# Kernel optimization log

Measured on AMD Instinct MI355X. Metric: run time of the kernel, lower is better.

Reference implementation:

```python
import jax, jax.numpy as jnp
import numpy as np

D_EMBED = 1024
N_HEADS = 16
D_HEAD = 64
D_MLP = 4096
SEQ = 2048
BATCH = 2
ALPHA = 1.0


def setup_inputs() -> dict:
    key = jax.random.key(0)
    ks = jax.random.split(key, 7)
    s = ALPHA / np.sqrt(D_EMBED)
    return {
        "x": jax.random.normal(ks[0], (BATCH, SEQ, D_EMBED), jnp.float32),
        "W_K": s * jax.random.normal(ks[1], (N_HEADS, D_HEAD, D_EMBED), jnp.float32),
        "W_Q": s * jax.random.normal(ks[2], (N_HEADS, D_HEAD, D_EMBED), jnp.float32),
        "W_V": s * jax.random.normal(ks[3], (N_HEADS, D_HEAD, D_EMBED), jnp.float32),
        "W_O": s * jax.random.normal(ks[4], (D_EMBED, N_HEADS * D_HEAD), jnp.float32),
        "W_in": s * jax.random.normal(ks[5], (D_MLP, D_EMBED), jnp.float32),
        "b_in": jnp.zeros((D_MLP,), jnp.float32),
        "W_out": s * jax.random.normal(ks[6], (D_EMBED, D_MLP), jnp.float32),
        "b_out": jnp.zeros((D_EMBED,), jnp.float32),
    }


def reference(x, W_K, W_Q, W_V, W_O, W_in, b_in, W_out, b_out):
    b, c_len, _ = x.shape
    d_head = W_K.shape[1]
    # q/k/v: [batch, head, ctx, d_head]
    k = jnp.einsum('ahe,bce->bach', W_K, x)
    q = jnp.einsum('ahe,bce->bach', W_Q, x)
    v = jnp.einsum('ahe,bce->bach', W_V, x)
    # scores[b,a,c,C] = k_c . q_C  (faithful to original index convention)
    scores = jnp.einsum('bach,baCh->bacC', k, q)
    mask = jnp.tril(jnp.ones((c_len, c_len), dtype=x.dtype))  # [c, C]
    masked = scores * mask - 1e10 * (1.0 - mask)
    attn = jax.nn.softmax(masked / np.sqrt(d_head), axis=-1)  # softmax over C (query idx)
    # z[b,a,C,h] = sum_c v[b,a,c,h] * attn[b,a,c,C]
    z = jnp.einsum('bach,bacC->baCh', v, attn)
    z_flat = jnp.transpose(z, (0, 2, 1, 3)).reshape(b, c_len, -1)  # [b, c, a*h]
    attn_out = jnp.einsum('ef,bcf->bce', W_O, z_flat)
    x = x + attn_out
    h = jnp.einsum('me,bce->bcm', W_in, x) + b_in
    h = jax.nn.relu(h)
    mlp_out = jnp.einsum('em,bcm->bce', W_out, h) + b_out
    return x + mlp_out
```

## Files before the change

kernel.cpp:

```cpp
#include <hip/hip_runtime.h>
#include <hip/hip_bf16.h>
#include <cstdint>
#include <cstddef>

typedef __bf16 bf16;
typedef bf16 bf16x4 __attribute__((ext_vector_type(4)));
typedef bf16 bf16x8 __attribute__((ext_vector_type(8)));
typedef float floatx4 __attribute__((ext_vector_type(4)));

#define MFMA16(a, b, c) __builtin_amdgcn_mfma_f32_16x16x32_bf16((a), (b), (c), 0, 0, 0)

#define K2 0.18033688011112042f

__device__ __forceinline__ void async16(const void* g, void* l) {
    __builtin_amdgcn_global_load_lds((const __attribute__((address_space(1))) void*)g,
                                     (__attribute__((address_space(3))) void*)l,
                                     16, 0, 0);
}

__device__ __forceinline__ void stage64(const bf16* g0, int ldg, bf16* lds, int wave, int lane) {
#pragma unroll
    for (int i = 0; i < 2; ++i) {
        int r0 = wave * 16 + i * 8;
        async16(g0 + (size_t)(r0 + (lane >> 3)) * ldg + (lane & 7) * 8,
                lds + r0 * 64);
    }
}

#define BAR_VM()                                              \
    do {                                                      \
        asm volatile("s_waitcnt vmcnt(0)" ::: "memory");      \
        __builtin_amdgcn_s_barrier();                         \
    } while (0)
#define BAR_LGKM()                                            \
    do {                                                      \
        asm volatile("s_waitcnt lgkmcnt(0)" ::: "memory");    \
        __builtin_amdgcn_s_barrier();                         \
    } while (0)

__global__ __launch_bounds__(256) void cvt_all(const float* __restrict__ x,
                                               const float* __restrict__ WQ,
                                               const float* __restrict__ WK,
                                               const float* __restrict__ WV,
                                               const float* __restrict__ WO,
                                               const float* __restrict__ Win,
                                               const float* __restrict__ Wout,
                                               bf16* __restrict__ xb,
                                               bf16* __restrict__ wqkv,
                                               bf16* __restrict__ wo,
                                               bf16* __restrict__ win,
                                               bf16* __restrict__ wout) {
    int blk = blockIdx.x;
    const float* src;
    bf16* dst;
    int off;
    if (blk < 1024)      { src = WQ;   dst = wqkv;           off = blk; }
    else if (blk < 2048) { src = WK;   dst = wqkv + 1048576; off = blk - 1024; }
    else if (blk < 3072) { src = WV;   dst = wqkv + 2097152; off = blk - 2048; }
    else if (blk < 4096) { src = WO;   dst = wo;             off = blk - 3072; }
    else if (blk < 8192) { src = Win;  dst = win;            off = blk - 4096; }
    else if (blk < 12288){ src = Wout; dst = wout;           off = blk - 8192; }
    else                 { src = x;    dst = xb;             off = blk - 12288; }
    int i = off * 1024 + threadIdx.x * 4;
    float4 v = *(const float4*)(src + i);
    bf16x4 o = {(bf16)v.x, (bf16)v.y, (bf16)v.z, (bf16)v.w};
    *(bf16x4*)(dst + i) = o;
}

template <int EPI, int NT>
__global__ __launch_bounds__(256) void gemm_dbuf(const bf16* __restrict__ A, int lda,
                                                 const bf16* __restrict__ B, int ldb, int K,
                                                 float* __restrict__ Cf, bf16* __restrict__ Cb,
                                                 int ldc, const float* __restrict__ bias,
                                                 const float* __restrict__ res) {
    constexpr int NACC = NT / 32;
    __shared__ __align__(16) bf16 As[2][128 * 32];
    __shared__ __align__(16) bf16 Bs[2][NT * 32];
    const int tid = threadIdx.x, wave = tid >> 6, lane = tid & 63;
    const int m0 = blockIdx.y * 128, n0 = blockIdx.x * NT;
    const int wm = (wave >> 1) * 64, wn = (wave & 1) * (NT / 2);
    const int col = lane & 15, quad = lane >> 4;

    floatx4 acc[4][NACC];
#pragma unroll
    for (int mi = 0; mi < 4; ++mi)
#pragma unroll
        for (int ni = 0; ni < NACC; ++ni) acc[mi][ni] = (floatx4){0.f, 0.f, 0.f, 0.f};

    auto stage = [&](int buf, int k0) {
#pragma unroll
        for (int i = 0; i < 2; ++i) {
            int r0 = wave * 32 + i * 16;
            async16(A + (size_t)(m0 + r0 + (lane >> 2)) * lda + k0 + (lane & 3) * 8,
                    As[buf] + r0 * 32);
        }
        if constexpr (NT == 128) {
#pragma unroll
            for (int i = 0; i < 2; ++i) {
                int r0 = wave * 32 + i * 16;
                async16(B + (size_t)(n0 + r0 + (lane >> 2)) * ldb + k0 + (lane & 3) * 8,
                        Bs[buf] + r0 * 32);
            }
        } else {
            int r0 = wave * 16;
            async16(B + (size_t)(n0 + r0 + (lane >> 2)) * ldb + k0 + (lane & 3) * 8,
                    Bs[buf] + r0 * 32);
        }
    };

    stage(0, 0);
    const int nk = K / 32;
    for (int it = 0; it < nk; ++it) {
        __syncthreads();
        if (it + 1 < nk) stage((it + 1) & 1, (it + 1) * 32);
        const int cur = it & 1;
        bf16x8 af[4], bfr[NACC];
#pragma unroll
        for (int mi = 0; mi < 4; ++mi)
            af[mi] = *(const bf16x8*)&As[cur][(wm + mi * 16 + col) * 32 + quad * 8];
#pragma unroll
        for (int ni = 0; ni < NACC; ++ni)
            bfr[ni] = *(const bf16x8*)&Bs[cur][(wn + ni * 16 + col) * 32 + quad * 8];
#pragma unroll
        for (int mi = 0; mi < 4; ++mi)
#pragma unroll
            for (int ni = 0; ni < NACC; ++ni)
                acc[mi][ni] = MFMA16(af[mi], bfr[ni], acc[mi][ni]);
    }

#pragma unroll
    for (int mi = 0; mi < 4; ++mi)
#pragma unroll
        for (int ni = 0; ni < NACC; ++ni)
#pragma unroll
            for (int r = 0; r < 4; ++r) {
                int row = m0 + wm + mi * 16 + quad * 4 + r;
                int cc = n0 + wn + ni * 16 + col;
                size_t idx = (size_t)row * ldc + cc;
                float v = acc[mi][ni][r];
                if constexpr (EPI == 0) {
                    Cb[idx] = (bf16)v;
                } else if constexpr (EPI == 1) {
                    v += res[idx];
                    Cf[idx] = v;
                    Cb[idx] = (bf16)v;
                } else if constexpr (EPI == 2) {
                    v += bias[cc];
                    v = fmaxf(v, 0.f);
                    Cb[idx] = (bf16)v;
                } else {
                    v += bias[cc] + Cf[idx];
                    Cf[idx] = v;
                }
            }
}

__global__ __launch_bounds__(256) void transpose_v(const bf16* __restrict__ qkv,
                                                   bf16* __restrict__ vt) {
    __shared__ bf16 t[64][65];
    const int bh = blockIdx.y, ct = blockIdx.x;
    const int b = bh >> 4, a = bh & 15;
    for (int idx = threadIdx.x; idx < 4096; idx += 256) {
        int c = idx >> 6, h = idx & 63;
        t[h][c] = qkv[(size_t)(b * 2048 + ct * 64 + c) * 3072 + 2048 + a * 64 + h];
    }
    __syncthreads();
    for (int idx = threadIdx.x; idx < 4096; idx += 256) {
        int h = idx >> 6, c = idx & 63;
        vt[(size_t)(bh * 64 + h) * 2048 + ct * 64 + c] = t[h][c];
    }
}

__global__ __launch_bounds__(256) void attn_stats(const bf16* __restrict__ qkv,
                                                  float* __restrict__ mp2) {
    __shared__ __align__(16) bf16 Kt[64 * 64];
    __shared__ __align__(16) bf16 Qt[2][64 * 64];
    const int xx = blockIdx.x;
    const int ct = (xx & 1) ? (31 - (xx >> 1)) : (xx >> 1);
    const int bh = blockIdx.y;
    const int b = bh >> 4, a = bh & 15;
    const int tid = threadIdx.x, wave = tid >> 6, lane = tid & 63;
    const int col = lane & 15, quad = lane >> 4;
    const bf16* base = qkv + (size_t)b * 2048 * 3072;

    stage64(base + (size_t)ct * 64 * 3072 + 1024 + a * 64, 3072, Kt, wave, lane);
    stage64(base + a * 64, 3072, Qt[0], wave, lane);

    float lrun[4] = {0.f, 0.f, 0.f, 0.f};
    bf16x8 a0, a1;

    for (int Ct = 0; Ct <= ct; ++Ct) {
        __syncthreads();
        if (Ct < ct)
            stage64(base + (size_t)(Ct + 1) * 64 * 3072 + a * 64, 3072,
                    Qt[(Ct + 1) & 1], wave, lane);
        if (Ct == 0) {
            a0 = *(const bf16x8*)&Kt[(wave * 16 + col) * 64 + quad * 8];
            a1 = *(const bf16x8*)&Kt[(wave * 16 + col) * 64 + 32 + quad * 8];
        }
        const bf16* q = Qt[Ct & 1];
#pragma unroll
        for (int nt = 0; nt < 4; ++nt) {
            bf16x8 b0 = *(const bf16x8*)&q[(nt * 16 + col) * 64 + quad * 8];
            bf16x8 b1 = *(const bf16x8*)&q[(nt * 16 + col) * 64 + 32 + quad * 8];
            floatx4 sacc = (floatx4){0.f, 0.f, 0.f, 0.f};
            sacc = MFMA16(a0, b0, sacc);
            sacc = MFMA16(a1, b1, sacc);
#pragma unroll
            for (int r = 0; r < 4; ++r) {
                float e = __builtin_amdgcn_exp2f(sacc[r] * K2);
                if (Ct == ct && (nt * 16 + col) > (wave * 16 + quad * 4 + r)) e = 0.f;
                lrun[r] += e;
            }
        }
    }
#pragma unroll
    for (int r = 0; r < 4; ++r) {
        float t = lrun[r];
        t += __shfl_xor(t, 1);
        t += __shfl_xor(t, 2);
        t += __shfl_xor(t, 4);
        t += __shfl_xor(t, 8);
        lrun[r] = t;
    }
    if (col == 0) {
#pragma unroll
        for (int r = 0; r < 4; ++r) {
            int c = ct * 64 + wave * 16 + quad * 4 + r;
            mp2[(size_t)bh * 2048 + c] = __builtin_amdgcn_logf(lrun[r]);
        }
    }
}

__global__ __launch_bounds__(256) void attn_av(const bf16* __restrict__ qkv,
                                               const bf16* __restrict__ vt,
                                               const float* __restrict__ mp2,
                                               bf16* __restrict__ zb) {
    __shared__ __align__(16) bf16 Qt[64 * 64];
    __shared__ __align__(16) bf16 Kt[2][64 * 64];
    __shared__ __align__(16) bf16 Vt[2][64 * 64];
    __shared__ __align__(16) bf16 Pt[64 * 72];
    const int xx = blockIdx.x;
    const int Ctile = (xx & 1) ? (31 - (xx >> 1)) : (xx >> 1);
    const int bh = blockIdx.y;
    const int b = bh >> 4, a = bh & 15;
    const int tid = threadIdx.x, wave = tid >> 6, lane = tid & 63;
    const int col = lane & 15, quad = lane >> 4;
    const bf16* base = qkv + (size_t)b * 2048 * 3072;
    const float* mpb = mp2 + (size_t)bh * 2048;

    stage64(base + (size_t)Ctile * 64 * 3072 + a * 64, 3072, Qt, wave, lane);
    stage64(base + (size_t)Ctile * 64 * 3072 + 1024 + a * 64, 3072, Kt[0], wave, lane);
    stage64(vt + (size_t)bh * 64 * 2048 + Ctile * 64, 2048, Vt[0], wave, lane);

    float4 mp_cur = *(const float4*)&mpb[Ctile * 64 + wave * 16 + quad * 4];

    floatx4 zacc[4];
#pragma unroll
    for (int mi = 0; mi < 4; ++mi) zacc[mi] = (floatx4){0.f, 0.f, 0.f, 0.f};
    bf16x8 qf0[4], qf1[4];

    for (int ct = Ctile; ct < 32; ++ct) {
        const int cur = (ct - Ctile) & 1;
        BAR_VM();
        if (ct + 1 < 32) {
            stage64(base + (size_t)(ct + 1) * 64 * 3072 + 1024 + a * 64, 3072,
                    Kt[cur ^ 1], wave, lane);
            stage64(vt + (size_t)bh * 64 * 2048 + (ct + 1) * 64, 2048,
                    Vt[cur ^ 1], wave, lane);
        }
        if (ct == Ctile) {
#pragma unroll
            for (int nt = 0; nt < 4; ++nt) {
                qf0[nt] = *(const bf16x8*)&Qt[(nt * 16 + col) * 64 + quad * 8];
                qf1[nt] = *(const bf16x8*)&Qt[(nt * 16 + col) * 64 + 32 + quad * 8];
            }
        }
        bf16x8 a0 = *(const bf16x8*)&Kt[cur][(wave * 16 + col) * 64 + quad * 8];
        bf16x8 a1 = *(const bf16x8*)&Kt[cur][(wave * 16 + col) * 64 + 32 + quad * 8];

        const float mpl[4] = {mp_cur.x, mp_cur.y, mp_cur.z, mp_cur.w};
#pragma unroll
        for (int nt = 0; nt < 4; ++nt) {
            floatx4 sacc = (floatx4){0.f, 0.f, 0.f, 0.f};
            sacc = MFMA16(a0, qf0[nt], sacc);
            sacc = MFMA16(a1, qf1[nt], sacc);
            bf16x4 pv;
#pragma unroll
            for (int r = 0; r < 4; ++r) {
                float p;
                if (ct == Ctile && (nt * 16 + col) > (wave * 16 + quad * 4 + r))
                    p = 0.f;
                else
                    p = __builtin_amdgcn_exp2f(sacc[r] * K2 - mpl[r]);
                pv[r] = (bf16)p;
            }
            *(bf16x4*)&Pt[(nt * 16 + col) * 72 + wave * 16 + quad * 4] = pv;
        }
        BAR_LGKM();

        float4 mp_nxt = mp_cur;
        if (ct + 1 < 32)
            mp_nxt = *(const float4*)&mpb[(ct + 1) * 64 + wave * 16 + quad * 4];

        bf16x8 v0 = *(const bf16x8*)&Vt[cur][(wave * 16 + col) * 64 + quad * 8];
        bf16x8 v1 = *(const bf16x8*)&Vt[cur][(wave * 16 + col) * 64 + 32 + quad * 8];
#pragma unroll
        for (int mi = 0; mi < 4; ++mi) {
            bf16x8 p0 = *(const bf16x8*)&Pt[(mi * 16 + col) * 72 + quad * 8];
            bf16x8 p1 = *(const bf16x8*)&Pt[(mi * 16 + col) * 72 + 32 + quad * 8];
            zacc[mi] = MFMA16(p0, v0, zacc[mi]);
            zacc[mi] = MFMA16(p1, v1, zacc[mi]);
        }
        mp_cur = mp_nxt;
    }
#pragma unroll
    for (int mi = 0; mi < 4; ++mi)
#pragma unroll
        for (int r = 0; r < 4; ++r) {
            int Cg = Ctile * 64 + mi * 16 + quad * 4 + r;
            zb[(size_t)(b * 2048 + Cg) * 1024 + a * 64 + wave * 16 + col] =
                (bf16)zacc[mi][r];
        }
}

extern "C" void kernel_launch(void* const* d_in, const int* in_sizes, int n_in,
                              void* d_out, int out_size, void* d_ws, size_t ws_size,
                              hipStream_t stream) {
    (void)in_sizes; (void)n_in; (void)out_size; (void)ws_size;
    const float* x    = (const float*)d_in[0];
    const float* WK   = (const float*)d_in[1];
    const float* WQ   = (const float*)d_in[2];
    const float* WV   = (const float*)d_in[3];
    const float* WO   = (const float*)d_in[4];
    const float* Win  = (const float*)d_in[5];
    const float* bin  = (const float*)d_in[6];
    const float* Wout = (const float*)d_in[7];
    const float* bout = (const float*)d_in[8];
    float* out = (float*)d_out;

    char* ws = (char*)d_ws;
    bf16*  xb   = (bf16*)(ws + 0);
    bf16*  wqkv = (bf16*)(ws + 8388608);
    bf16*  wo   = (bf16*)(ws + 14680064);
    bf16*  win  = (bf16*)(ws + 16777216);
    bf16*  wout = (bf16*)(ws + 25165824);
    bf16*  qkvb = (bf16*)(ws + 33554432);
    bf16*  vtb  = (bf16*)(ws + 58720256);
    float* mst  = (float*)(ws + 67108864);
    bf16*  zbuf = (bf16*)(ws + 67633152);
    bf16*  xmid = (bf16*)(ws + 76021760);
    bf16*  hbuf = (bf16*)(ws + 84410368);

    cvt_all<<<16384, 256, 0, stream>>>(x, WQ, WK, WV, WO, Win, Wout,
                                       xb, wqkv, wo, win, wout);

    gemm_dbuf<0, 128><<<dim3(24, 32), 256, 0, stream>>>(xb, 1024, wqkv, 1024, 1024,
                                                        nullptr, qkvb, 3072, nullptr, nullptr);
    transpose_v<<<dim3(32, 32), 256, 0, stream>>>(qkvb, vtb);
    attn_stats<<<dim3(32, 32), 256, 0, stream>>>(qkvb, mst);
    attn_av<<<dim3(32, 32), 256, 0, stream>>>(qkvb, vtb, mst, zbuf);
    gemm_dbuf<1, 64><<<dim3(16, 32), 256, 0, stream>>>(zbuf, 1024, wo, 1024, 1024,
                                                       out, xmid, 1024, nullptr, x);
    gemm_dbuf<2, 128><<<dim3(32, 32), 256, 0, stream>>>(xmid, 1024, win, 1024, 1024,
                                                        nullptr, hbuf, 4096, bin, nullptr);
    gemm_dbuf<3, 64><<<dim3(16, 32), 256, 0, stream>>>(hbuf, 4096, wout, 4096, 4096,
                                                       out, nullptr, 1024, bout, nullptr);
}
```

Measured before the change: 419.1 us.

## Triple-buffer GEMM and attention loads with XOR-swizzled LDS and vmcnt waits

Moves the GEMM and both attention kernels from double to triple buffering. Loads are issued two stages ahead and gated with partial s_waitcnt vmcnt counts instead of full syncs, so global-to-LDS copies overlap more compute. LDS tiles get an XOR swizzle on the global source column, matched in the reads, to cut bank conflicts. attn_av also stages its per-row stats into LDS up front rather than loading them per iteration. The trade is more LDS per block, which may lower occupancy, and fragile hand-counted wait values.

```diff
diff --git a/kernel.cpp b/kernel.cpp
--- a/kernel.cpp
+++ b/kernel.cpp
@@ -18,25 +18,20 @@
                                      16, 0, 0);
 }
 
-__device__ __forceinline__ void stage64(const bf16* g0, int ldg, bf16* lds, int wave, int lane) {
+__device__ __forceinline__ void stage64s(const bf16* g0, int ldg, bf16* lds, int wave, int lane) {
 #pragma unroll
     for (int i = 0; i < 2; ++i) {
         int r0 = wave * 16 + i * 8;
-        async16(g0 + (size_t)(r0 + (lane >> 3)) * ldg + (lane & 7) * 8,
+        async16(g0 + (size_t)(r0 + (lane >> 3)) * ldg + ((lane & 7) ^ (lane >> 3)) * 8,
                 lds + r0 * 64);
     }
 }
-
-#define BAR_VM()                                              \
-    do {                                                      \
-        asm volatile("s_waitcnt vmcnt(0)" ::: "memory");      \
-        __builtin_amdgcn_s_barrier();                         \
-    } while (0)
-#define BAR_LGKM()                                            \
-    do {                                                      \
-        asm volatile("s_waitcnt lgkmcnt(0)" ::: "memory");    \
-        __builtin_amdgcn_s_barrier();                         \
-    } while (0)
+__device__ __forceinline__ bf16x8 rd64(const bf16* t, int row, int chunk) {
+    return *(const bf16x8*)&t[row * 64 + ((chunk ^ (row & 7)) * 8)];
+}
+__device__ __forceinline__ bf16x8 rd32(const bf16* t, int row, int quad) {
+    return *(const bf16x8*)&t[row * 32 + ((quad ^ (row & 3)) * 8)];
+}
 
 __global__ __launch_bounds__(256) void cvt_all(const float* __restrict__ x,
                                                const float* __restrict__ WQ,
@@ -68,18 +63,19 @@
 }
 
 template <int EPI, int NT>
-__global__ __launch_bounds__(256) void gemm_dbuf(const bf16* __restrict__ A, int lda,
+__global__ __launch_bounds__(256) void gemm_pipe(const bf16* __restrict__ A, int lda,
                                                  const bf16* __restrict__ B, int ldb, int K,
                                                  float* __restrict__ Cf, bf16* __restrict__ Cb,
                                                  int ldc, const float* __restrict__ bias,
                                                  const float* __restrict__ res) {
     constexpr int NACC = NT / 32;
-    __shared__ __align__(16) bf16 As[2][128 * 32];
-    __shared__ __align__(16) bf16 Bs[2][NT * 32];
+    __shared__ __align__(16) bf16 As[3][128 * 32];
+    __shared__ __align__(16) bf16 Bs[3][NT * 32];
     const int tid = threadIdx.x, wave = tid >> 6, lane = tid & 63;
     const int m0 = blockIdx.y * 128, n0 = blockIdx.x * NT;
     const int wm = (wave >> 1) * 64, wn = (wave & 1) * (NT / 2);
     const int col = lane & 15, quad = lane >> 4;
+    const int cs8 = ((lane & 3) ^ ((lane >> 2) & 3)) * 8;
 
     floatx4 acc[4][NACC];
 #pragma unroll
@@ -91,36 +87,43 @@
 #pragma unroll
         for (int i = 0; i < 2; ++i) {
             int r0 = wave * 32 + i * 16;
-            async16(A + (size_t)(m0 + r0 + (lane >> 2)) * lda + k0 + (lane & 3) * 8,
+            async16(A + (size_t)(m0 + r0 + (lane >> 2)) * lda + k0 + cs8,
                     As[buf] + r0 * 32);
         }
         if constexpr (NT == 128) {
 #pragma unroll
             for (int i = 0; i < 2; ++i) {
                 int r0 = wave * 32 + i * 16;
-                async16(B + (size_t)(n0 + r0 + (lane >> 2)) * ldb + k0 + (lane & 3) * 8,
+                async16(B + (size_t)(n0 + r0 + (lane >> 2)) * ldb + k0 + cs8,
                         Bs[buf] + r0 * 32);
             }
         } else {
             int r0 = wave * 16;
-            async16(B + (size_t)(n0 + r0 + (lane >> 2)) * ldb + k0 + (lane & 3) * 8,
+            async16(B + (size_t)(n0 + r0 + (lane >> 2)) * ldb + k0 + cs8,
                     Bs[buf] + r0 * 32);
         }
     };
 
+    const int nk = K / 32;
     stage(0, 0);
-    const int nk = K / 32;
+    stage(1, 32);
     for (int it = 0; it < nk; ++it) {
-        __syncthreads();
-        if (it + 1 < nk) stage((it + 1) & 1, (it + 1) * 32);
-        const int cur = it & 1;
+        if (it + 1 < nk) {
+            if constexpr (NT == 128) asm volatile("s_waitcnt vmcnt(4)" ::: "memory");
+            else                     asm volatile("s_waitcnt vmcnt(3)" ::: "memory");
+        } else {
+            asm volatile("s_waitcnt vmcnt(0)" ::: "memory");
+        }
+        __builtin_amdgcn_s_barrier();
+        if (it + 2 < nk) stage((it + 2) % 3, (it + 2) * 32);
+
+        const bf16* as = As[it % 3];
+        const bf16* bs = Bs[it % 3];
         bf16x8 af[4], bfr[NACC];
 #pragma unroll
-        for (int mi = 0; mi < 4; ++mi)
-            af[mi] = *(const bf16x8*)&As[cur][(wm + mi * 16 + col) * 32 + quad * 8];
-#pragma unroll
-        for (int ni = 0; ni < NACC; ++ni)
-            bfr[ni] = *(const bf16x8*)&Bs[cur][(wn + ni * 16 + col) * 32 + quad * 8];
+        for (int mi = 0; mi < 4; ++mi) af[mi] = rd32(as, wm + mi * 16 + col, quad);
+#pragma unroll
+        for (int ni = 0; ni < NACC; ++ni) bfr[ni] = rd32(bs, wn + ni * 16 + col, quad);
 #pragma unroll
         for (int mi = 0; mi < 4; ++mi)
 #pragma unroll
@@ -174,7 +177,7 @@
 __global__ __launch_bounds__(256) void attn_stats(const bf16* __restrict__ qkv,
                                                   float* __restrict__ mp2) {
     __shared__ __align__(16) bf16 Kt[64 * 64];
-    __shared__ __align__(16) bf16 Qt[2][64 * 64];
+    __shared__ __align__(16) bf16 Qt[3][64 * 64];
     const int xx = blockIdx.x;
     const int ct = (xx & 1) ? (31 - (xx >> 1)) : (xx >> 1);
     const int bh = blockIdx.y;
@@ -183,26 +186,29 @@
     const int col = lane & 15, quad = lane >> 4;
     const bf16* base = qkv + (size_t)b * 2048 * 3072;
 
-    stage64(base + (size_t)ct * 64 * 3072 + 1024 + a * 64, 3072, Kt, wave, lane);
-    stage64(base + a * 64, 3072, Qt[0], wave, lane);
+    stage64s(base + (size_t)ct * 64 * 3072 + 1024 + a * 64, 3072, Kt, wave, lane);
+    stage64s(base + a * 64, 3072, Qt[0], wave, lane);
+    if (ct >= 1) stage64s(base + (size_t)1 * 64 * 3072 + a * 64, 3072, Qt[1], wave, lane);
 
     float lrun[4] = {0.f, 0.f, 0.f, 0.f};
     bf16x8 a0, a1;
 
     for (int Ct = 0; Ct <= ct; ++Ct) {
-        __syncthreads();
-        if (Ct < ct)
-            stage64(base + (size_t)(Ct + 1) * 64 * 3072 + a * 64, 3072,
-                    Qt[(Ct + 1) & 1], wave, lane);
+        if (Ct < ct) asm volatile("s_waitcnt vmcnt(2)" ::: "memory");
+        else         asm volatile("s_waitcnt vmcnt(0)" ::: "memory");
+        __builtin_amdgcn_s_barrier();
+        if (Ct + 2 <= ct)
+            stage64s(base + (size_t)(Ct + 2) * 64 * 3072 + a * 64, 3072,
+                     Qt[(Ct + 2) % 3], wave, lane);
         if (Ct == 0) {
-            a0 = *(const bf16x8*)&Kt[(wave * 16 + col) * 64 + quad * 8];
-            a1 = *(const bf16x8*)&Kt[(wave * 16 + col) * 64 + 32 + quad * 8];
-        }
-        const bf16* q = Qt[Ct & 1];
+            a0 = rd64(Kt, wave * 16 + col, quad);
+            a1 = rd64(Kt, wave * 16 + col, quad + 4);
+        }
+        const bf16* q = Qt[Ct % 3];
 #pragma unroll
         for (int nt = 0; nt < 4; ++nt) {
-            bf16x8 b0 = *(const bf16x8*)&q[(nt * 16 + col) * 64 + quad * 8];
-            bf16x8 b1 = *(const bf16x8*)&q[(nt * 16 + col) * 64 + 32 + quad * 8];
+            bf16x8 b0 = rd64(q, nt * 16 + col, quad);
+            bf16x8 b1 = rd64(q, nt * 16 + col, quad + 4);
             floatx4 sacc = (floatx4){0.f, 0.f, 0.f, 0.f};
             sacc = MFMA16(a0, b0, sacc);
             sacc = MFMA16(a1, b1, sacc);
@@ -237,9 +243,10 @@
                                                const float* __restrict__ mp2,
                                                bf16* __restrict__ zb) {
     __shared__ __align__(16) bf16 Qt[64 * 64];
-    __shared__ __align__(16) bf16 Kt[2][64 * 64];
-    __shared__ __align__(16) bf16 Vt[2][64 * 64];
+    __shared__ __align__(16) bf16 Kt[3][64 * 64];
+    __shared__ __align__(16) bf16 Vt[3][64 * 64];
     __shared__ __align__(16) bf16 Pt[64 * 72];
+    __shared__ __align__(16) float mpS[2048];
     const int xx = blockIdx.x;
     const int Ctile = (xx & 1) ? (31 - (xx >> 1)) : (xx >> 1);
     const int bh = blockIdx.y;
@@ -248,38 +255,56 @@
     const int col = lane & 15, quad = lane >> 4;
     const bf16* base = qkv + (size_t)b * 2048 * 3072;
     const float* mpb = mp2 + (size_t)bh * 2048;
-
-    stage64(base + (size_t)Ctile * 64 * 3072 + a * 64, 3072, Qt, wave, lane);
-    stage64(base + (size_t)Ctile * 64 * 3072 + 1024 + a * 64, 3072, Kt[0], wave, lane);
-    stage64(vt + (size_t)bh * 64 * 2048 + Ctile * 64, 2048, Vt[0], wave, lane);
-
-    float4 mp_cur = *(const float4*)&mpb[Ctile * 64 + wave * 16 + quad * 4];
+    const int niter = 32 - Ctile;
+
+    stage64s(base + (size_t)Ctile * 64 * 3072 + a * 64, 3072, Qt, wave, lane);
+    {
+        int nb = niter * 256;
+#pragma unroll
+        for (int i = 0; i < 2; ++i) {
+            int off = (i * 4 + wave) * 1024;
+            if (off < nb)
+                async16((const char*)(mpb + Ctile * 64) + off + lane * 16,
+                        (char*)mpS + off);
+        }
+    }
+    stage64s(base + (size_t)Ctile * 64 * 3072 + 1024 + a * 64, 3072, Kt[0], wave, lane);
+    stage64s(vt + (size_t)bh * 64 * 2048 + Ctile * 64, 2048, Vt[0], wave, lane);
+    if (niter > 1) {
+        stage64s(base + (size_t)(Ctile + 1) * 64 * 3072 + 1024 + a * 64, 3072, Kt[1], wave, lane);
+        stage64s(vt + (size_t)bh * 64 * 2048 + (Ctile + 1) * 64, 2048, Vt[1], wave, lane);
+    }
 
     floatx4 zacc[4];
 #pragma unroll
     for (int mi = 0; mi < 4; ++mi) zacc[mi] = (floatx4){0.f, 0.f, 0.f, 0.f};
     bf16x8 qf0[4], qf1[4];
 
-    for (int ct = Ctile; ct < 32; ++ct) {
-        const int cur = (ct - Ctile) & 1;
-        BAR_VM();
-        if (ct + 1 < 32) {
-            stage64(base + (size_t)(ct + 1) * 64 * 3072 + 1024 + a * 64, 3072,
-                    Kt[cur ^ 1], wave, lane);
-            stage64(vt + (size_t)bh * 64 * 2048 + (ct + 1) * 64, 2048,
-                    Vt[cur ^ 1], wave, lane);
-        }
-        if (ct == Ctile) {
+    for (int i = 0; i < niter; ++i) {
+        const int ct = Ctile + i;
+        if (i + 1 < niter) asm volatile("s_waitcnt vmcnt(4)" ::: "memory");
+        else               asm volatile("s_waitcnt vmcnt(0)" ::: "memory");
+        __builtin_amdgcn_s_barrier();
+        if (i + 2 < niter) {
+            stage64s(base + (size_t)(ct + 2) * 64 * 3072 + 1024 + a * 64, 3072,
+                     Kt[(i + 2) % 3], wave, lane);
+            stage64s(vt + (size_t)bh * 64 * 2048 + (ct + 2) * 64, 2048,
+                     Vt[(i + 2) % 3], wave, lane);
+        }
+        if (i == 0) {
 #pragma unroll
             for (int nt = 0; nt < 4; ++nt) {
-                qf0[nt] = *(const bf16x8*)&Qt[(nt * 16 + col) * 64 + quad * 8];
-                qf1[nt] = *(const bf16x8*)&Qt[(nt * 16 + col) * 64 + 32 + quad * 8];
-            }
-        }
-        bf16x8 a0 = *(const bf16x8*)&Kt[cur][(wave * 16 + col) * 64 + quad * 8];
-        bf16x8 a1 = *(const bf16x8*)&Kt[cur][(wave * 16 + col) * 64 + 32 + quad * 8];
-
-        const float mpl[4] = {mp_cur.x, mp_cur.y, mp_cur.z, mp_cur.w};
+                qf0[nt] = rd64(Qt, nt * 16 + col, quad);
+                qf1[nt] = rd64(Qt, nt * 16 + col, quad + 4);
+            }
+        }
+        const bf16* kt = Kt[i % 3];
+        const bf16* vts = Vt[i % 3];
+        bf16x8 a0 = rd64(kt, wave * 16 + col, quad);
+        bf16x8 a1 = rd64(kt, wave * 16 + col, quad + 4);
+        float4 mpv = *(const float4*)&mpS[i * 64 + wave * 16 + quad * 4];
+        const float mpl[4] = {mpv.x, mpv.y, mpv.z, mpv.w};
+
 #pragma unroll
         for (int nt = 0; nt < 4; ++nt) {
             floatx4 sacc = (floatx4){0.f, 0.f, 0.f, 0.f};
@@ -297,14 +322,11 @@
             }
             *(bf16x4*)&Pt[(nt * 16 + col) * 72 + wave * 16 + quad * 4] = pv;
         }
-        BAR_LGKM();
-
-        float4 mp_nxt = mp_cur;
-        if (ct + 1 < 32)
-            mp_nxt = *(const float4*)&mpb[(ct + 1) * 64 + wave * 16 + quad * 4];
-
-        bf16x8 v0 = *(const bf16x8*)&Vt[cur][(wave * 16 + col) * 64 + quad * 8];
-        bf16x8 v1 = *(const bf16x8*)&Vt[cur][(wave * 16 + col) * 64 + 32 + quad * 8];
+        asm volatile("s_waitcnt lgkmcnt(0)" ::: "memory");
+        __builtin_amdgcn_s_barrier();
+
+        bf16x8 v0 = rd64(vts, wave * 16 + col, quad);
+        bf16x8 v1 = rd64(vts, wave * 16 + col, quad + 4);
 #pragma unroll
         for (int mi = 0; mi < 4; ++mi) {
             bf16x8 p0 = *(const bf16x8*)&Pt[(mi * 16 + col) * 72 + quad * 8];
@@ -312,7 +334,6 @@
             zacc[mi] = MFMA16(p0, v0, zacc[mi]);
             zacc[mi] = MFMA16(p1, v1, zacc[mi]);
         }
-        mp_cur = mp_nxt;
     }
 #pragma unroll
     for (int mi = 0; mi < 4; ++mi)
@@ -355,15 +376,15 @@
     cvt_all<<<16384, 256, 0, stream>>>(x, WQ, WK, WV, WO, Win, Wout,
                                        xb, wqkv, wo, win, wout);
 
-    gemm_dbuf<0, 128><<<dim3(24, 32), 256, 0, stream>>>(xb, 1024, wqkv, 1024, 1024,
+    gemm_pipe<0, 128><<<dim3(24, 32), 256, 0, stream>>>(xb, 1024, wqkv, 1024, 1024,
                                                         nullptr, qkvb, 3072, nullptr, nullptr);
     transpose_v<<<dim3(32, 32), 256, 0, stream>>>(qkvb, vtb);
     attn_stats<<<dim3(32, 32), 256, 0, stream>>>(qkvb, mst);
     attn_av<<<dim3(32, 32), 256, 0, stream>>>(qkvb, vtb, mst, zbuf);
-    gemm_dbuf<1, 64><<<dim3(16, 32), 256, 0, stream>>>(zbuf, 1024, wo, 1024, 1024,
+    gemm_pipe<1, 64><<<dim3(16, 32), 256, 0, stream>>>(zbuf, 1024, wo, 1024, 1024,
                                                        out, xmid, 1024, nullptr, x);
-    gemm_dbuf<2, 128><<<dim3(32, 32), 256, 0, stream>>>(xmid, 1024, win, 1024, 1024,
+    gemm_pipe<2, 128><<<dim3(32, 32), 256, 0, stream>>>(xmid, 1024, win, 1024, 1024,
                                                         nullptr, hbuf, 4096, bin, nullptr);
-    gemm_dbuf<3, 64><<<dim3(16, 32), 256, 0, stream>>>(hbuf, 4096, wout, 4096, 4096,
+    gemm_pipe<3, 64><<<dim3(16, 32), 256, 0, stream>>>(hbuf, 4096, wout, 4096, 4096,
                                                        out, nullptr, 1024, bout, nullptr);
 }
```

After: 410.4 us. 1.02x faster.
